# Performance work log

Measured on AMD Instinct MI355X. Metric: run time of the kernel, lower is better.

## Reference

```python
import jax, jax.numpy as jnp
import numpy as np

EPS = 1e-8  # torch CosineSimilarity eps


def setup_inputs() -> dict:
    key = jax.random.key(0)
    ks = jax.random.split(key, 7)
    B, N, T, C, M, MEM, IN, E = 8, 512, 64, 128, 32, 20, 2, 4
    s = 0.05  # keep softmax logits in a sane range (xavier-like scale)
    return {
        "input": jax.random.normal(ks[0], (B, N, T, IN), jnp.float32),
        "hidden": jax.random.normal(ks[1], (E, B, N, T, C), jnp.float32),
        "memory": jax.random.normal(ks[2], (MEM, M), jnp.float32) * s,
        "input_query": jax.random.normal(ks[3], (IN, M), jnp.float32) * s,
        "Wq": jax.random.normal(ks[4], (E, C, M), jnp.float32) * s,
        "Wk": jax.random.normal(ks[5], (E, C, M), jnp.float32) * s,
        "Wv": jax.random.normal(ks[6], (E, C, M), jnp.float32) * s,
    }


def _cosine_sim(a, b):
    # torch.nn.CosineSimilarity(dim=-1): dot / (max(||a||,eps)*max(||b||,eps))
    num = jnp.sum(a * b, axis=-1)
    na = jnp.maximum(jnp.linalg.norm(a, axis=-1), EPS)
    nb = jnp.maximum(jnp.linalg.norm(b, axis=-1), EPS)
    return num / (na * nb)


def reference(input, hidden, memory, input_query, Wq, Wk, Wv):
    B, N, T, _ = input.shape
    out_dim = 1
    # query_mem: soft read from memory bank -> [B,N,T,mem_hid]
    q_in = jnp.einsum("bnti,im->bntm", input, input_query)
    mem_score = jax.nn.softmax(jnp.einsum("bntm,km->bntk", q_in, memory), axis=-1)
    memories = jnp.einsum("bntk,km->bntm", mem_score, memory)
    # per-expert self-attention over T (vectorized over the 4 experts)
    q = jnp.einsum("ebntc,ecm->ebntm", hidden, Wq)
    k = jnp.einsum("ebntc,ecm->ebntm", hidden, Wk)
    v = jnp.einsum("ebntc,ecm->ebntm", hidden, Wv)
    energy = jnp.einsum("ebntm,ebnsm->ebnts", q, k)  # [E,B,N,T,T]
    att = jnp.einsum("ebnts,ebnsm->ebntm", jax.nn.softmax(energy, axis=-1), v)
    # cosine similarity of memory read vs each expert's attended hidden
    scores = _cosine_sim(memories[None], att)  # [E,B,N,T]
    scores = jnp.moveaxis(scores, 0, -1)  # [B,N,T,E]
    out = jnp.broadcast_to(scores[..., None, :], (B, N, T, out_dim, scores.shape[-1]))
    return out
```

## Files before the change

kernel.cpp:

```cpp
#include <hip/hip_runtime.h>
#include <hip/hip_bf16.h>
#include <math.h>

#define Bc 8
#define Nc 512
#define Tc 64
#define Cc 128
#define Mc 32
#define MEMc 20
#define Ec 4

#define LDK  40
#define LDVT 72

typedef short bf16x8 __attribute__((ext_vector_type(8)));
typedef float f32x4  __attribute__((ext_vector_type(4)));

__device__ __forceinline__ unsigned short f2bfu(float f) {
    return __builtin_bit_cast(unsigned short, __float2bfloat16(f));
}
__device__ __forceinline__ unsigned pk2bf(float x, float y) {
    return ((unsigned)f2bfu(y) << 16) | (unsigned)f2bfu(x);
}

__device__ __forceinline__ void gload_lds16(const void* g, void* l) {
    __builtin_amdgcn_global_load_lds(
        (const __attribute__((address_space(1))) unsigned int*)g,
        (__attribute__((address_space(3))) unsigned int*)l, 16, 0, 0);
}

__global__ void prep(const float* __restrict__ Wq, const float* __restrict__ Wk,
                     const float* __restrict__ Wv, const float* __restrict__ membank,
                     const float* __restrict__ iq,
                     short* __restrict__ wt_img, short* __restrict__ bankM,
                     float* __restrict__ G2) {
    const int t = threadIdx.x;
    if (blockIdx.x < 192) {
        int idx = blockIdx.x * 256 + t;
        int e   = idx / 12288;
        int r   = idx - e * 12288;
        int mat = r >> 12;
        int m   = (r >> 7) & 31;
        int c   = r & 127;
        const float* W = (mat == 0) ? Wq : (mat == 1) ? Wk : Wv;
        const int dst = e * 12288 + mat * 4096 + m * 128 + (c ^ ((m & 7) << 3));
        wt_img[dst] = (short)f2bfu(W[((size_t)e * Cc + c) * Mc + m]);
    } else {
        for (int idx = t; idx < Mc * 32; idx += 256) {
            int m = idx >> 5, k = idx & 31;
            bankM[idx] = (short)f2bfu((k < MEMc) ? membank[k * Mc + m] : 0.f);
        }
        if (t < MEMc) {
            float g0 = 0.f, g1 = 0.f;
            for (int m = 0; m < Mc; ++m) {
                float b = membank[t * Mc + m];
                g0 = fmaf(iq[m], b, g0);
                g1 = fmaf(iq[Mc + m], b, g1);
            }
            G2[2 * t]     = g0;
            G2[2 * t + 1] = g1;
        }
    }
}

__global__ __launch_bounds__(256, 3) void mg_mfma(
    const float* __restrict__ input,
    const float* __restrict__ hidden,
    const short* __restrict__ wt_img,
    const short* __restrict__ bankM,
    const float* __restrict__ G2,
    float* __restrict__ out)
{
    __shared__ __align__(16) short sh_wt[12288];
    __shared__ __align__(16) short sh_k [2][Tc * LDK];
    __shared__ __align__(16) short sh_vt[2][Mc * LDVT];

    const int t    = threadIdx.x;
    const int w    = t >> 6;
    const int lane = t & 63;
    const int lo   = lane & 15;
    const int hi   = lane >> 4;
    const int e    = blockIdx.x >> 11;
    const int bn0  = (blockIdx.x & 2047) * 2;
    const int bn1  = bn0 + 1;

    {
        const short* gsrc = wt_img + (size_t)e * 12288 + w * 512 + lane * 8;
        short* ldst = sh_wt + w * 512;
        #pragma unroll
        for (int c = 0; c < 6; ++c)
            gload_lds16(gsrc + c * 2048, ldst + c * 2048);
    }

    const float2 in2_0 = *(const float2*)(input + ((size_t)bn0 * Tc + lane) * 2);
    const float2 in2_1 = *(const float2*)(input + ((size_t)bn1 * Tc + lane) * 2);
    float4 h0[8], h1[8];
    {
        const float* hr0 = hidden + (((size_t)(e * 4096 + bn0)) * Tc + w * 16 + lo) * Cc + hi * 8;
        const float* hr1 = hidden + (((size_t)(e * 4096 + bn1)) * Tc + w * 16 + lo) * Cc + hi * 8;
        #pragma unroll
        for (int kt = 0; kt < 4; ++kt) {
            h0[2 * kt]     = *(const float4*)(hr0 + kt * 32);
            h0[2 * kt + 1] = *(const float4*)(hr0 + kt * 32 + 4);
            h1[2 * kt]     = *(const float4*)(hr1 + kt * 32);
            h1[2 * kt + 1] = *(const float4*)(hr1 + kt * 32 + 4);
        }
    }

    unsigned pd0[10], pd1[10];
    #pragma unroll
    for (int kp = 0; kp < 10; ++kp) {
        const float4 g = *(const float4*)(G2 + 4 * kp);
        pd0[kp] = pk2bf(__expf(in2_0.x * g.x + in2_0.y * g.y),
                        __expf(in2_0.x * g.z + in2_0.y * g.w));
        pd1[kp] = pk2bf(__expf(in2_1.x * g.x + in2_1.y * g.y),
                        __expf(in2_1.x * g.z + in2_1.y * g.w));
    }

    f32x4 am0[2], am1[2];
    am0[0] = am0[1] = (f32x4){0.f, 0.f, 0.f, 0.f};
    am1[0] = am1[1] = (f32x4){0.f, 0.f, 0.f, 0.f};
    {
        const int addrD = (w * 16 + lo) * 4;
        unsigned W0[10], W1[10];
        #pragma unroll
        for (int u = 0; u < 10; ++u) {
            W0[u] = __builtin_amdgcn_ds_bpermute(addrD, (int)pd0[u]);
            W1[u] = __builtin_amdgcn_ds_bpermute(addrD, (int)pd1[u]);
        }
        unsigned b0[4], b1[4];
        #pragma unroll
        for (int u = 0; u < 4; ++u) {
            const unsigned l0 = (hi == 0) ? W0[u] : W0[4 + u];
            const unsigned h0_ = (u < 2) ? ((hi == 2) ? W0[8 + u] : 0u) : 0u;
            b0[u] = (hi < 2) ? l0 : h0_;
            const unsigned l1 = (hi == 0) ? W1[u] : W1[4 + u];
            const unsigned h1_ = (u < 2) ? ((hi == 2) ? W1[8 + u] : 0u) : 0u;
            b1[u] = (hi < 2) ? l1 : h1_;
        }
        const bf16x8 bp20 = __builtin_bit_cast(bf16x8, (uint4){b0[0], b0[1], b0[2], b0[3]});
        const bf16x8 bp21 = __builtin_bit_cast(bf16x8, (uint4){b1[0], b1[1], b1[2], b1[3]});
        #pragma unroll
        for (int nt = 0; nt < 2; ++nt) {
            const bf16x8 ab = *(const bf16x8*)(bankM + (nt * 16 + lo) * 32 + hi * 8);
            am0[nt] = __builtin_amdgcn_mfma_f32_16x16x32_bf16(ab, bp20, am0[nt], 0, 0, 0);
            am1[nt] = __builtin_amdgcn_mfma_f32_16x16x32_bf16(ab, bp21, am1[nt], 0, 0, 0);
        }
    }

    bf16x8 a0[4], a1[4];
    #pragma unroll
    for (int kt = 0; kt < 4; ++kt) {
        const float4 x0 = h0[2 * kt], y0 = h0[2 * kt + 1];
        a0[kt] = __builtin_bit_cast(bf16x8, (uint4){pk2bf(x0.x, x0.y), pk2bf(x0.z, x0.w),
                                                    pk2bf(y0.x, y0.y), pk2bf(y0.z, y0.w)});
        const float4 x1 = h1[2 * kt], y1 = h1[2 * kt + 1];
        a1[kt] = __builtin_bit_cast(bf16x8, (uint4){pk2bf(x1.x, x1.y), pk2bf(x1.z, x1.w),
                                                    pk2bf(y1.x, y1.y), pk2bf(y1.z, y1.w)});
    }

    __syncthreads();

    f32x4 q0_[2], k0_[2], v0_[2], q1_[2], k1_[2], v1_[2];
    #pragma unroll
    for (int nt = 0; nt < 2; ++nt) {
        q0_[nt] = k0_[nt] = v0_[nt] = (f32x4){0.f, 0.f, 0.f, 0.f};
        q1_[nt] = k1_[nt] = v1_[nt] = (f32x4){0.f, 0.f, 0.f, 0.f};
    }
    {
        const int swz = (lo & 7) << 3;
        int col[4];
        #pragma unroll
        for (int kt = 0; kt < 4; ++kt) col[kt] = (kt * 32 + hi * 8) ^ swz;
        const short* wrow = sh_wt + lo * 128;
        #pragma unroll
        for (int nt = 0; nt < 2; ++nt) {
            const short* p0 = wrow + nt * 2048;
            #pragma unroll
            for (int kt = 0; kt < 4; ++kt) {
                const bf16x8 wq = *(const bf16x8*)(p0 + col[kt]);
                const bf16x8 wk = *(const bf16x8*)(p0 + 4096 + col[kt]);
                const bf16x8 wv = *(const bf16x8*)(p0 + 8192 + col[kt]);
                q0_[nt] = __builtin_amdgcn_mfma_f32_16x16x32_bf16(wq, a0[kt], q0_[nt], 0, 0, 0);
                k0_[nt] = __builtin_amdgcn_mfma_f32_16x16x32_bf16(wk, a0[kt], k0_[nt], 0, 0, 0);
                v0_[nt] = __builtin_amdgcn_mfma_f32_16x16x32_bf16(wv, a0[kt], v0_[nt], 0, 0, 0);
                q1_[nt] = __builtin_amdgcn_mfma_f32_16x16x32_bf16(wq, a1[kt], q1_[nt], 0, 0, 0);
                k1_[nt] = __builtin_amdgcn_mfma_f32_16x16x32_bf16(wk, a1[kt], k1_[nt], 0, 0, 0);
                v1_[nt] = __builtin_amdgcn_mfma_f32_16x16x32_bf16(wv, a1[kt], v1_[nt], 0, 0, 0);
            }
        }
    }
    unsigned q_pk0[4], q_pk1[4];
    #pragma unroll
    for (int nt = 0; nt < 2; ++nt) {
        *(uint2*)&sh_k[0][(w * 16 + lo) * LDK + nt * 16 + hi * 4] =
            (uint2){pk2bf(k0_[nt][0], k0_[nt][1]), pk2bf(k0_[nt][2], k0_[nt][3])};
        *(uint2*)&sh_k[1][(w * 16 + lo) * LDK + nt * 16 + hi * 4] =
            (uint2){pk2bf(k1_[nt][0], k1_[nt][1]), pk2bf(k1_[nt][2], k1_[nt][3])};
        #pragma unroll
        for (int j = 0; j < 4; ++j) {
            sh_vt[0][(nt * 16 + hi * 4 + j) * LDVT + w * 16 + lo] = (short)f2bfu(v0_[nt][j]);
            sh_vt[1][(nt * 16 + hi * 4 + j) * LDVT + w * 16 + lo] = (short)f2bfu(v1_[nt][j]);
        }
        q_pk0[nt * 2]     = pk2bf(q0_[nt][0], q0_[nt][1]);
        q_pk0[nt * 2 + 1] = pk2bf(q0_[nt][2], q0_[nt][3]);
        q_pk1[nt * 2]     = pk2bf(q1_[nt][0], q1_[nt][1]);
        q_pk1[nt * 2 + 1] = pk2bf(q1_[nt][2], q1_[nt][3]);
    }

    __syncthreads();

    const int A01   = (((hi & 1) * 32) + lo) << 2;
    const int A23   = A01 + 64;
    const int addrA = (((hi & 1) * 2 + 0) * 16 + lo) * 4;
    const int addrB = (((hi & 1) * 2 + 1) * 16 + lo) * 4;

    #pragma unroll
    for (int u = 0; u < 2; ++u) {
        const unsigned* q_pk = u ? q_pk1 : q_pk0;
        const f32x4*    am   = u ? am1   : am0;
        const int       bn   = u ? bn1   : bn0;

        unsigned pw[4][2];
        {
            unsigned l0 = __builtin_amdgcn_ds_bpermute(A01, (int)q_pk[0]);
            unsigned h0_ = __builtin_amdgcn_ds_bpermute(A01, (int)q_pk[2]);
            unsigned l1 = __builtin_amdgcn_ds_bpermute(A01, (int)q_pk[1]);
            unsigned h1_ = __builtin_amdgcn_ds_bpermute(A01, (int)q_pk[3]);
            unsigned l2 = __builtin_amdgcn_ds_bpermute(A23, (int)q_pk[0]);
            unsigned h2_ = __builtin_amdgcn_ds_bpermute(A23, (int)q_pk[2]);
            unsigned l3 = __builtin_amdgcn_ds_bpermute(A23, (int)q_pk[1]);
            unsigned h3_ = __builtin_amdgcn_ds_bpermute(A23, (int)q_pk[3]);
            const bf16x8 bq = __builtin_bit_cast(bf16x8, (uint4){
                (hi < 2) ? l0 : h0_, (hi < 2) ? l1 : h1_,
                (hi < 2) ? l2 : h2_, (hi < 2) ? l3 : h3_});
            #pragma unroll
            for (int st = 0; st < 4; ++st) {
                const bf16x8 akf = *(const bf16x8*)&sh_k[u][(st * 16 + lo) * LDK + hi * 8];
                const f32x4 en = __builtin_amdgcn_mfma_f32_16x16x32_bf16(
                    akf, bq, (f32x4){0.f, 0.f, 0.f, 0.f}, 0, 0, 0);
                pw[st][0] = pk2bf(__expf(en[0]), __expf(en[1]));
                pw[st][1] = pk2bf(__expf(en[2]), __expf(en[3]));
            }
        }

        f32x4 av[2];
        av[0] = av[1] = (f32x4){0.f, 0.f, 0.f, 0.f};
        {
            bf16x8 bp[2];
            #pragma unroll
            for (int kt = 0; kt < 2; ++kt) {
                unsigned wrd[4];
                #pragma unroll
                for (int uu = 0; uu < 4; ++uu) {
                    const int adr = (uu < 2) ? addrA : addrB;
                    const unsigned ev = __builtin_amdgcn_ds_bpermute(adr, (int)pw[2 * kt][uu & 1]);
                    const unsigned od = __builtin_amdgcn_ds_bpermute(adr, (int)pw[2 * kt + 1][uu & 1]);
                    wrd[uu] = (hi < 2) ? ev : od;
                }
                bp[kt] = __builtin_bit_cast(bf16x8, (uint4){wrd[0], wrd[1], wrd[2], wrd[3]});
            }
            #pragma unroll
            for (int nt = 0; nt < 2; ++nt)
                #pragma unroll
                for (int kt = 0; kt < 2; ++kt) {
                    const bf16x8 avt = *(const bf16x8*)&sh_vt[u][(nt * 16 + lo) * LDVT + kt * 32 + hi * 8];
                    av[nt] = __builtin_amdgcn_mfma_f32_16x16x32_bf16(avt, bp[kt], av[nt], 0, 0, 0);
                }
        }

        float d = 0.f, na = 0.f, nb = 0.f;
        #pragma unroll
        for (int nt = 0; nt < 2; ++nt)
            #pragma unroll
            for (int j = 0; j < 4; ++j) {
                const float av_ = av[nt][j], am_ = am[nt][j];
                d  = fmaf(av_, am_, d);
                na = fmaf(av_, av_, na);
                nb = fmaf(am_, am_, nb);
            }
        d  += __shfl_xor(d, 16);  d  += __shfl_xor(d, 32);
        na += __shfl_xor(na, 16); na += __shfl_xor(na, 32);
        nb += __shfl_xor(nb, 16); nb += __shfl_xor(nb, 32);
        if (hi == 0) {
            const float denom = fmaxf(sqrtf(na), 1e-8f) * fmaxf(sqrtf(nb), 1e-8f);
            out[((size_t)bn * Tc + w * 16 + lo) * Ec + e] = d / denom;
        }
    }
}

extern "C" void kernel_launch(void* const* d_in, const int* in_sizes, int n_in,
                              void* d_out, int out_size, void* d_ws, size_t ws_size,
                              hipStream_t stream) {
    const float* input   = (const float*)d_in[0];
    const float* hidden  = (const float*)d_in[1];
    const float* membank = (const float*)d_in[2];
    const float* iq      = (const float*)d_in[3];
    const float* Wq      = (const float*)d_in[4];
    const float* Wk      = (const float*)d_in[5];
    const float* Wv      = (const float*)d_in[6];
    float* out = (float*)d_out;

    short* wt_img = (short*)d_ws;
    short* bankM  = (short*)((char*)d_ws + 98304);
    float* G2     = (float*)((char*)d_ws + 100352);

    prep<<<193, 256, 0, stream>>>(Wq, Wk, Wv, membank, iq, wt_img, bankM, G2);
    mg_mfma<<<Ec * Bc * Nc / 2, 256, 0, stream>>>(input, hidden, wt_img, bankM, G2, out);
}
```

Before: 122.8 us.

## Serialize the two row pairs per block, prefetching second hidden during first attention

Each block now processes its two (b,n) rows one after another instead of together. The K/V LDS buffers drop to a single copy and register pressure roughly halves, so launch bounds rise from 3 to 4 blocks per SM. The second row's hidden load and memory read are issued before the first row's attention, so the global latency overlaps with that compute. In exchange the kernel adds two extra __syncthreads, and the row-pair MFMA interleaving that hid latency within a wave is lost.

```diff
diff --git a/kernel.cpp b/kernel.cpp
--- a/kernel.cpp
+++ b/kernel.cpp
@@ -63,7 +63,136 @@
     }
 }
 
-__global__ __launch_bounds__(256, 3) void mg_mfma(
+__device__ __forceinline__ void proj(const short* __restrict__ sh_wt, const bf16x8* a,
+                                     int lo, int hi,
+                                     f32x4 q_[2], f32x4 k_[2], f32x4 v_[2]) {
+    #pragma unroll
+    for (int nt = 0; nt < 2; ++nt)
+        q_[nt] = k_[nt] = v_[nt] = (f32x4){0.f, 0.f, 0.f, 0.f};
+    const int swz = (lo & 7) << 3;
+    int col[4];
+    #pragma unroll
+    for (int kt = 0; kt < 4; ++kt) col[kt] = (kt * 32 + hi * 8) ^ swz;
+    const short* wrow = sh_wt + lo * 128;
+    #pragma unroll
+    for (int nt = 0; nt < 2; ++nt) {
+        const short* p0 = wrow + nt * 2048;
+        #pragma unroll
+        for (int kt = 0; kt < 4; ++kt) {
+            const bf16x8 wq = *(const bf16x8*)(p0 + col[kt]);
+            const bf16x8 wk = *(const bf16x8*)(p0 + 4096 + col[kt]);
+            const bf16x8 wv = *(const bf16x8*)(p0 + 8192 + col[kt]);
+            q_[nt] = __builtin_amdgcn_mfma_f32_16x16x32_bf16(wq, a[kt], q_[nt], 0, 0, 0);
+            k_[nt] = __builtin_amdgcn_mfma_f32_16x16x32_bf16(wk, a[kt], k_[nt], 0, 0, 0);
+            v_[nt] = __builtin_amdgcn_mfma_f32_16x16x32_bf16(wv, a[kt], v_[nt], 0, 0, 0);
+        }
+    }
+}
+
+__device__ __forceinline__ void gate_pd(const float* __restrict__ G2, float2 in2, unsigned pd[10]) {
+    #pragma unroll
+    for (int kp = 0; kp < 10; ++kp) {
+        const float4 g = *(const float4*)(G2 + 4 * kp);
+        pd[kp] = pk2bf(__expf(in2.x * g.x + in2.y * g.y),
+                       __expf(in2.x * g.z + in2.y * g.w));
+    }
+}
+
+__device__ __forceinline__ void mem_read(const short* __restrict__ bankM,
+                                         const unsigned pd[10], int lo, int hi, int w,
+                                         f32x4 am[2]) {
+    am[0] = am[1] = (f32x4){0.f, 0.f, 0.f, 0.f};
+    const int addrD = (w * 16 + lo) * 4;
+    unsigned Wd[10];
+    #pragma unroll
+    for (int u = 0; u < 10; ++u)
+        Wd[u] = __builtin_amdgcn_ds_bpermute(addrD, (int)pd[u]);
+    unsigned b[4];
+    #pragma unroll
+    for (int u = 0; u < 4; ++u) {
+        const unsigned l_ = (hi == 0) ? Wd[u] : Wd[4 + u];
+        const unsigned h_ = (u < 2) ? ((hi == 2) ? Wd[8 + u] : 0u) : 0u;
+        b[u] = (hi < 2) ? l_ : h_;
+    }
+    const bf16x8 bp2 = __builtin_bit_cast(bf16x8, (uint4){b[0], b[1], b[2], b[3]});
+    #pragma unroll
+    for (int nt = 0; nt < 2; ++nt) {
+        const bf16x8 ab = *(const bf16x8*)(bankM + (nt * 16 + lo) * 32 + hi * 8);
+        am[nt] = __builtin_amdgcn_mfma_f32_16x16x32_bf16(ab, bp2, am[nt], 0, 0, 0);
+    }
+}
+
+__device__ __forceinline__ void attend_store(
+    const short* __restrict__ shk, const short* __restrict__ shv,
+    const unsigned q_pk[4], const f32x4 am[2],
+    int lo, int hi, int w, int A01, int A23, int addrA, int addrB,
+    int bn, int e, float* __restrict__ out) {
+    unsigned pw[4][2];
+    {
+        unsigned l0 = __builtin_amdgcn_ds_bpermute(A01, (int)q_pk[0]);
+        unsigned h0_ = __builtin_amdgcn_ds_bpermute(A01, (int)q_pk[2]);
+        unsigned l1 = __builtin_amdgcn_ds_bpermute(A01, (int)q_pk[1]);
+        unsigned h1_ = __builtin_amdgcn_ds_bpermute(A01, (int)q_pk[3]);
+        unsigned l2 = __builtin_amdgcn_ds_bpermute(A23, (int)q_pk[0]);
+        unsigned h2_ = __builtin_amdgcn_ds_bpermute(A23, (int)q_pk[2]);
+        unsigned l3 = __builtin_amdgcn_ds_bpermute(A23, (int)q_pk[1]);
+        unsigned h3_ = __builtin_amdgcn_ds_bpermute(A23, (int)q_pk[3]);
+        const bf16x8 bq = __builtin_bit_cast(bf16x8, (uint4){
+            (hi < 2) ? l0 : h0_, (hi < 2) ? l1 : h1_,
+            (hi < 2) ? l2 : h2_, (hi < 2) ? l3 : h3_});
+        #pragma unroll
+        for (int st = 0; st < 4; ++st) {
+            const bf16x8 akf = *(const bf16x8*)&shk[(st * 16 + lo) * LDK + hi * 8];
+            const f32x4 en = __builtin_amdgcn_mfma_f32_16x16x32_bf16(
+                akf, bq, (f32x4){0.f, 0.f, 0.f, 0.f}, 0, 0, 0);
+            pw[st][0] = pk2bf(__expf(en[0]), __expf(en[1]));
+            pw[st][1] = pk2bf(__expf(en[2]), __expf(en[3]));
+        }
+    }
+    f32x4 av[2];
+    av[0] = av[1] = (f32x4){0.f, 0.f, 0.f, 0.f};
+    {
+        bf16x8 bp[2];
+        #pragma unroll
+        for (int kt = 0; kt < 2; ++kt) {
+            unsigned wrd[4];
+            #pragma unroll
+            for (int uu = 0; uu < 4; ++uu) {
+                const int adr = (uu < 2) ? addrA : addrB;
+                const unsigned ev = __builtin_amdgcn_ds_bpermute(adr, (int)pw[2 * kt][uu & 1]);
+                const unsigned od = __builtin_amdgcn_ds_bpermute(adr, (int)pw[2 * kt + 1][uu & 1]);
+                wrd[uu] = (hi < 2) ? ev : od;
+            }
+            bp[kt] = __builtin_bit_cast(bf16x8, (uint4){wrd[0], wrd[1], wrd[2], wrd[3]});
+        }
+        #pragma unroll
+        for (int nt = 0; nt < 2; ++nt)
+            #pragma unroll
+            for (int kt = 0; kt < 2; ++kt) {
+                const bf16x8 avt = *(const bf16x8*)&shv[(nt * 16 + lo) * LDVT + kt * 32 + hi * 8];
+                av[nt] = __builtin_amdgcn_mfma_f32_16x16x32_bf16(avt, bp[kt], av[nt], 0, 0, 0);
+            }
+    }
+    float d = 0.f, na = 0.f, nb = 0.f;
+    #pragma unroll
+    for (int nt = 0; nt < 2; ++nt)
+        #pragma unroll
+        for (int j = 0; j < 4; ++j) {
+            const float av_ = av[nt][j], am_ = am[nt][j];
+            d  = fmaf(av_, am_, d);
+            na = fmaf(av_, av_, na);
+            nb = fmaf(am_, am_, nb);
+        }
+    d  += __shfl_xor(d, 16);  d  += __shfl_xor(d, 32);
+    na += __shfl_xor(na, 16); na += __shfl_xor(na, 32);
+    nb += __shfl_xor(nb, 16); nb += __shfl_xor(nb, 32);
+    if (hi == 0) {
+        const float denom = fmaxf(sqrtf(na), 1e-8f) * fmaxf(sqrtf(nb), 1e-8f);
+        out[((size_t)bn * Tc + w * 16 + lo) * Ec + e] = d / denom;
+    }
+}
+
+__global__ __launch_bounds__(256, 4) void mg_mfma(
     const float* __restrict__ input,
     const float* __restrict__ hidden,
     const short* __restrict__ wt_img,
@@ -72,8 +201,8 @@
     float* __restrict__ out)
 {
     __shared__ __align__(16) short sh_wt[12288];
-    __shared__ __align__(16) short sh_k [2][Tc * LDK];
-    __shared__ __align__(16) short sh_vt[2][Mc * LDVT];
+    __shared__ __align__(16) short sh_k [Tc * LDK];
+    __shared__ __align__(16) short sh_vt[Mc * LDVT];
 
     const int t    = threadIdx.x;
     const int w    = t >> 6;
@@ -84,209 +213,113 @@
     const int bn0  = (blockIdx.x & 2047) * 2;
     const int bn1  = bn0 + 1;
 
-    {
-        const short* gsrc = wt_img + (size_t)e * 12288 + w * 512 + lane * 8;
-        short* ldst = sh_wt + w * 512;
-        #pragma unroll
-        for (int c = 0; c < 6; ++c)
-            gload_lds16(gsrc + c * 2048, ldst + c * 2048);
-    }
-
-    const float2 in2_0 = *(const float2*)(input + ((size_t)bn0 * Tc + lane) * 2);
-    const float2 in2_1 = *(const float2*)(input + ((size_t)bn1 * Tc + lane) * 2);
-    float4 h0[8], h1[8];
-    {
-        const float* hr0 = hidden + (((size_t)(e * 4096 + bn0)) * Tc + w * 16 + lo) * Cc + hi * 8;
-        const float* hr1 = hidden + (((size_t)(e * 4096 + bn1)) * Tc + w * 16 + lo) * Cc + hi * 8;
-        #pragma unroll
-        for (int kt = 0; kt < 4; ++kt) {
-            h0[2 * kt]     = *(const float4*)(hr0 + kt * 32);
-            h0[2 * kt + 1] = *(const float4*)(hr0 + kt * 32 + 4);
-            h1[2 * kt]     = *(const float4*)(hr1 + kt * 32);
-            h1[2 * kt + 1] = *(const float4*)(hr1 + kt * 32 + 4);
-        }
-    }
-
-    unsigned pd0[10], pd1[10];
-    #pragma unroll
-    for (int kp = 0; kp < 10; ++kp) {
-        const float4 g = *(const float4*)(G2 + 4 * kp);
-        pd0[kp] = pk2bf(__expf(in2_0.x * g.x + in2_0.y * g.y),
-                        __expf(in2_0.x * g.z + in2_0.y * g.w));
-        pd1[kp] = pk2bf(__expf(in2_1.x * g.x + in2_1.y * g.y),
-                        __expf(in2_1.x * g.z + in2_1.y * g.w));
-    }
-
-    f32x4 am0[2], am1[2];
-    am0[0] = am0[1] = (f32x4){0.f, 0.f, 0.f, 0.f};
-    am1[0] = am1[1] = (f32x4){0.f, 0.f, 0.f, 0.f};
-    {
-        const int addrD = (w * 16 + lo) * 4;
-        unsigned W0[10], W1[10];
-        #pragma unroll
-        for (int u = 0; u < 10; ++u) {
-            W0[u] = __builtin_amdgcn_ds_bpermute(addrD, (int)pd0[u]);
-            W1[u] = __builtin_amdgcn_ds_bpermute(addrD, (int)pd1[u]);
-        }
-        unsigned b0[4], b1[4];
-        #pragma unroll
-        for (int u = 0; u < 4; ++u) {
-            const unsigned l0 = (hi == 0) ? W0[u] : W0[4 + u];
-            const unsigned h0_ = (u < 2) ? ((hi == 2) ? W0[8 + u] : 0u) : 0u;
-            b0[u] = (hi < 2) ? l0 : h0_;
-            const unsigned l1 = (hi == 0) ? W1[u] : W1[4 + u];
-            const unsigned h1_ = (u < 2) ? ((hi == 2) ? W1[8 + u] : 0u) : 0u;
-            b1[u] = (hi < 2) ? l1 : h1_;
-        }
-        const bf16x8 bp20 = __builtin_bit_cast(bf16x8, (uint4){b0[0], b0[1], b0[2], b0[3]});
-        const bf16x8 bp21 = __builtin_bit_cast(bf16x8, (uint4){b1[0], b1[1], b1[2], b1[3]});
-        #pragma unroll
-        for (int nt = 0; nt < 2; ++nt) {
-            const bf16x8 ab = *(const bf16x8*)(bankM + (nt * 16 + lo) * 32 + hi * 8);
-            am0[nt] = __builtin_amdgcn_mfma_f32_16x16x32_bf16(ab, bp20, am0[nt], 0, 0, 0);
-            am1[nt] = __builtin_amdgcn_mfma_f32_16x16x32_bf16(ab, bp21, am1[nt], 0, 0, 0);
-        }
-    }
-
-    bf16x8 a0[4], a1[4];
-    #pragma unroll
-    for (int kt = 0; kt < 4; ++kt) {
-        const float4 x0 = h0[2 * kt], y0 = h0[2 * kt + 1];
-        a0[kt] = __builtin_bit_cast(bf16x8, (uint4){pk2bf(x0.x, x0.y), pk2bf(x0.z, x0.w),
-                                                    pk2bf(y0.x, y0.y), pk2bf(y0.z, y0.w)});
-        const float4 x1 = h1[2 * kt], y1 = h1[2 * kt + 1];
-        a1[kt] = __builtin_bit_cast(bf16x8, (uint4){pk2bf(x1.x, x1.y), pk2bf(x1.z, x1.w),
-                                                    pk2bf(y1.x, y1.y), pk2bf(y1.z, y1.w)});
-    }
-
-    __syncthreads();
-
-    f32x4 q0_[2], k0_[2], v0_[2], q1_[2], k1_[2], v1_[2];
-    #pragma unroll
-    for (int nt = 0; nt < 2; ++nt) {
-        q0_[nt] = k0_[nt] = v0_[nt] = (f32x4){0.f, 0.f, 0.f, 0.f};
-        q1_[nt] = k1_[nt] = v1_[nt] = (f32x4){0.f, 0.f, 0.f, 0.f};
-    }
-    {
-        const int swz = (lo & 7) << 3;
-        int col[4];
-        #pragma unroll
-        for (int kt = 0; kt < 4; ++kt) col[kt] = (kt * 32 + hi * 8) ^ swz;
-        const short* wrow = sh_wt + lo * 128;
-        #pragma unroll
-        for (int nt = 0; nt < 2; ++nt) {
-            const short* p0 = wrow + nt * 2048;
-            #pragma unroll
-            for (int kt = 0; kt < 4; ++kt) {
-                const bf16x8 wq = *(const bf16x8*)(p0 + col[kt]);
-                const bf16x8 wk = *(const bf16x8*)(p0 + 4096 + col[kt]);
-                const bf16x8 wv = *(const bf16x8*)(p0 + 8192 + col[kt]);
-                q0_[nt] = __builtin_amdgcn_mfma_f32_16x16x32_bf16(wq, a0[kt], q0_[nt], 0, 0, 0);
-                k0_[nt] = __builtin_amdgcn_mfma_f32_16x16x32_bf16(wk, a0[kt], k0_[nt], 0, 0, 0);
-                v0_[nt] = __builtin_amdgcn_mfma_f32_16x16x32_bf16(wv, a0[kt], v0_[nt], 0, 0, 0);
-                q1_[nt] = __builtin_amdgcn_mfma_f32_16x16x32_bf16(wq, a1[kt], q1_[nt], 0, 0, 0);
-                k1_[nt] = __builtin_amdgcn_mfma_f32_16x16x32_bf16(wk, a1[kt], k1_[nt], 0, 0, 0);
-                v1_[nt] = __builtin_amdgcn_mfma_f32_16x16x32_bf16(wv, a1[kt], v1_[nt], 0, 0, 0);
-            }
-        }
-    }
-    unsigned q_pk0[4], q_pk1[4];
-    #pragma unroll
-    for (int nt = 0; nt < 2; ++nt) {
-        *(uint2*)&sh_k[0][(w * 16 + lo) * LDK + nt * 16 + hi * 4] =
-            (uint2){pk2bf(k0_[nt][0], k0_[nt][1]), pk2bf(k0_[nt][2], k0_[nt][3])};
-        *(uint2*)&sh_k[1][(w * 16 + lo) * LDK + nt * 16 + hi * 4] =
-            (uint2){pk2bf(k1_[nt][0], k1_[nt][1]), pk2bf(k1_[nt][2], k1_[nt][3])};
-        #pragma unroll
-        for (int j = 0; j < 4; ++j) {
-            sh_vt[0][(nt * 16 + hi * 4 + j) * LDVT + w * 16 + lo] = (short)f2bfu(v0_[nt][j]);
-            sh_vt[1][(nt * 16 + hi * 4 + j) * LDVT + w * 16 + lo] = (short)f2bfu(v1_[nt][j]);
-        }
-        q_pk0[nt * 2]     = pk2bf(q0_[nt][0], q0_[nt][1]);
-        q_pk0[nt * 2 + 1] = pk2bf(q0_[nt][2], q0_[nt][3]);
-        q_pk1[nt * 2]     = pk2bf(q1_[nt][0], q1_[nt][1]);
-        q_pk1[nt * 2 + 1] = pk2bf(q1_[nt][2], q1_[nt][3]);
-    }
-
-    __syncthreads();
-
     const int A01   = (((hi & 1) * 32) + lo) << 2;
     const int A23   = A01 + 64;
     const int addrA = (((hi & 1) * 2 + 0) * 16 + lo) * 4;
     const int addrB = (((hi & 1) * 2 + 1) * 16 + lo) * 4;
 
-    #pragma unroll
-    for (int u = 0; u < 2; ++u) {
-        const unsigned* q_pk = u ? q_pk1 : q_pk0;
-        const f32x4*    am   = u ? am1   : am0;
-        const int       bn   = u ? bn1   : bn0;
-
-        unsigned pw[4][2];
-        {
-            unsigned l0 = __builtin_amdgcn_ds_bpermute(A01, (int)q_pk[0]);
-            unsigned h0_ = __builtin_amdgcn_ds_bpermute(A01, (int)q_pk[2]);
-            unsigned l1 = __builtin_amdgcn_ds_bpermute(A01, (int)q_pk[1]);
-            unsigned h1_ = __builtin_amdgcn_ds_bpermute(A01, (int)q_pk[3]);
-            unsigned l2 = __builtin_amdgcn_ds_bpermute(A23, (int)q_pk[0]);
-            unsigned h2_ = __builtin_amdgcn_ds_bpermute(A23, (int)q_pk[2]);
-            unsigned l3 = __builtin_amdgcn_ds_bpermute(A23, (int)q_pk[1]);
-            unsigned h3_ = __builtin_amdgcn_ds_bpermute(A23, (int)q_pk[3]);
-            const bf16x8 bq = __builtin_bit_cast(bf16x8, (uint4){
-                (hi < 2) ? l0 : h0_, (hi < 2) ? l1 : h1_,
-                (hi < 2) ? l2 : h2_, (hi < 2) ? l3 : h3_});
+    {
+        const short* gsrc = wt_img + (size_t)e * 12288 + w * 512 + lane * 8;
+        short* ldst = sh_wt + w * 512;
+        #pragma unroll
+        for (int c = 0; c < 6; ++c)
+            gload_lds16(gsrc + c * 2048, ldst + c * 2048);
+    }
+
+    const float2 in2_0 = *(const float2*)(input + ((size_t)bn0 * Tc + lane) * 2);
+    const float2 in2_1 = *(const float2*)(input + ((size_t)bn1 * Tc + lane) * 2);
+    float4 h[8];
+    {
+        const float* hr0 = hidden + (((size_t)(e * 4096 + bn0)) * Tc + w * 16 + lo) * Cc + hi * 8;
+        #pragma unroll
+        for (int kt = 0; kt < 4; ++kt) {
+            h[2 * kt]     = *(const float4*)(hr0 + kt * 32);
+            h[2 * kt + 1] = *(const float4*)(hr0 + kt * 32 + 4);
+        }
+    }
+
+    f32x4 am0[2];
+    {
+        unsigned pd0[10];
+        gate_pd(G2, in2_0, pd0);
+        mem_read(bankM, pd0, lo, hi, w, am0);
+    }
+
+    bf16x8 a0[4];
+    #pragma unroll
+    for (int kt = 0; kt < 4; ++kt) {
+        const float4 x = h[2 * kt], y = h[2 * kt + 1];
+        a0[kt] = __builtin_bit_cast(bf16x8, (uint4){pk2bf(x.x, x.y), pk2bf(x.z, x.w),
+                                                    pk2bf(y.x, y.y), pk2bf(y.z, y.w)});
+    }
+
+    __syncthreads();
+
+    unsigned q_pk0[4];
+    {
+        f32x4 q_[2], k_[2], v_[2];
+        proj(sh_wt, a0, lo, hi, q_, k_, v_);
+        #pragma unroll
+        for (int nt = 0; nt < 2; ++nt) {
+            *(uint2*)&sh_k[(w * 16 + lo) * LDK + nt * 16 + hi * 4] =
+                (uint2){pk2bf(k_[nt][0], k_[nt][1]), pk2bf(k_[nt][2], k_[nt][3])};
             #pragma unroll
-            for (int st = 0; st < 4; ++st) {
-                const bf16x8 akf = *(const bf16x8*)&sh_k[u][(st * 16 + lo) * LDK + hi * 8];
-                const f32x4 en = __builtin_amdgcn_mfma_f32_16x16x32_bf16(
-                    akf, bq, (f32x4){0.f, 0.f, 0.f, 0.f}, 0, 0, 0);
-                pw[st][0] = pk2bf(__expf(en[0]), __expf(en[1]));
-                pw[st][1] = pk2bf(__expf(en[2]), __expf(en[3]));
-            }
-        }
-
-        f32x4 av[2];
-        av[0] = av[1] = (f32x4){0.f, 0.f, 0.f, 0.f};
-        {
-            bf16x8 bp[2];
+            for (int j = 0; j < 4; ++j)
+                sh_vt[(nt * 16 + hi * 4 + j) * LDVT + w * 16 + lo] = (short)f2bfu(v_[nt][j]);
+            q_pk0[nt * 2]     = pk2bf(q_[nt][0], q_[nt][1]);
+            q_pk0[nt * 2 + 1] = pk2bf(q_[nt][2], q_[nt][3]);
+        }
+    }
+
+    __syncthreads();
+
+    {
+        const float* hr1 = hidden + (((size_t)(e * 4096 + bn1)) * Tc + w * 16 + lo) * Cc + hi * 8;
+        #pragma unroll
+        for (int kt = 0; kt < 4; ++kt) {
+            h[2 * kt]     = *(const float4*)(hr1 + kt * 32);
+            h[2 * kt + 1] = *(const float4*)(hr1 + kt * 32 + 4);
+        }
+    }
+
+    f32x4 am1[2];
+    {
+        unsigned pd1[10];
+        gate_pd(G2, in2_1, pd1);
+        mem_read(bankM, pd1, lo, hi, w, am1);
+    }
+
+    attend_store(sh_k, sh_vt, q_pk0, am0, lo, hi, w, A01, A23, addrA, addrB, bn0, e, out);
+
+    bf16x8 a1[4];
+    #pragma unroll
+    for (int kt = 0; kt < 4; ++kt) {
+        const float4 x = h[2 * kt], y = h[2 * kt + 1];
+        a1[kt] = __builtin_bit_cast(bf16x8, (uint4){pk2bf(x.x, x.y), pk2bf(x.z, x.w),
+                                                    pk2bf(y.x, y.y), pk2bf(y.z, y.w)});
+    }
+
+    __syncthreads();
+
+    unsigned q_pk1[4];
+    {
+        f32x4 q_[2], k_[2], v_[2];
+        proj(sh_wt, a1, lo, hi, q_, k_, v_);
+        #pragma unroll
+        for (int nt = 0; nt < 2; ++nt) {
+            *(uint2*)&sh_k[(w * 16 + lo) * LDK + nt * 16 + hi * 4] =
+                (uint2){pk2bf(k_[nt][0], k_[nt][1]), pk2bf(k_[nt][2], k_[nt][3])};
             #pragma unroll
-            for (int kt = 0; kt < 2; ++kt) {
-                unsigned wrd[4];
-                #pragma unroll
-                for (int uu = 0; uu < 4; ++uu) {
-                    const int adr = (uu < 2) ? addrA : addrB;
-                    const unsigned ev = __builtin_amdgcn_ds_bpermute(adr, (int)pw[2 * kt][uu & 1]);
-                    const unsigned od = __builtin_amdgcn_ds_bpermute(adr, (int)pw[2 * kt + 1][uu & 1]);
-                    wrd[uu] = (hi < 2) ? ev : od;
-                }
-                bp[kt] = __builtin_bit_cast(bf16x8, (uint4){wrd[0], wrd[1], wrd[2], wrd[3]});
-            }
-            #pragma unroll
-            for (int nt = 0; nt < 2; ++nt)
-                #pragma unroll
-                for (int kt = 0; kt < 2; ++kt) {
-                    const bf16x8 avt = *(const bf16x8*)&sh_vt[u][(nt * 16 + lo) * LDVT + kt * 32 + hi * 8];
-                    av[nt] = __builtin_amdgcn_mfma_f32_16x16x32_bf16(avt, bp[kt], av[nt], 0, 0, 0);
-                }
-        }
-
-        float d = 0.f, na = 0.f, nb = 0.f;
-        #pragma unroll
-        for (int nt = 0; nt < 2; ++nt)
-            #pragma unroll
-            for (int j = 0; j < 4; ++j) {
-                const float av_ = av[nt][j], am_ = am[nt][j];
-                d  = fmaf(av_, am_, d);
-                na = fmaf(av_, av_, na);
-                nb = fmaf(am_, am_, nb);
-            }
-        d  += __shfl_xor(d, 16);  d  += __shfl_xor(d, 32);
-        na += __shfl_xor(na, 16); na += __shfl_xor(na, 32);
-        nb += __shfl_xor(nb, 16); nb += __shfl_xor(nb, 32);
-        if (hi == 0) {
-            const float denom = fmaxf(sqrtf(na), 1e-8f) * fmaxf(sqrtf(nb), 1e-8f);
-            out[((size_t)bn * Tc + w * 16 + lo) * Ec + e] = d / denom;
-        }
-    }
+            for (int j = 0; j < 4; ++j)
+                sh_vt[(nt * 16 + hi * 4 + j) * LDVT + w * 16 + lo] = (short)f2bfu(v_[nt][j]);
+            q_pk1[nt * 2]     = pk2bf(q_[nt][0], q_[nt][1]);
+            q_pk1[nt * 2 + 1] = pk2bf(q_[nt][2], q_[nt][3]);
+        }
+    }
+
+    __syncthreads();
+
+    attend_store(sh_k, sh_vt, q_pk1, am1, lo, hi, w, A01, A23, addrA, addrB, bn1, e, out);
 }
 
 extern "C" void kernel_launch(void* const* d_in, const int* in_sizes, int n_in,
```

Measured after the change: 121.4 us, median of 2. No clear change (-1.1%).
